# Kernel optimization log

Hardware: AMD Instinct MI355X
Metric: run time of the kernel (lower is better)

Reference implementation:

```python
import jax, jax.numpy as jnp
import numpy as np

NUM_HEADS = 32
NUM_KV_HEADS = 8
HEAD_DIM = 64
GQA_GROUPS = NUM_HEADS // NUM_KV_HEADS
HIDDEN = 2048
B, S = 2, 2048


def setup_inputs() -> dict:
    key = jax.random.key(0)
    ks = jax.random.split(key, 7)
    scale = 1.0 / np.sqrt(HIDDEN)
    return {
        "x": jax.random.normal(ks[0], (B, S, HIDDEN), dtype=jnp.float32),
        "rotary_cos": jax.random.uniform(ks[1], (S, HEAD_DIM // 2), dtype=jnp.float32),
        "rotary_sin": jax.random.uniform(ks[2], (S, HEAD_DIM // 2), dtype=jnp.float32),
        "Wq": jax.random.normal(ks[3], (HIDDEN, NUM_HEADS * HEAD_DIM), dtype=jnp.float32) * scale,
        "Wk": jax.random.normal(ks[4], (HIDDEN, NUM_KV_HEADS * HEAD_DIM), dtype=jnp.float32) * scale,
        "Wv": jax.random.normal(ks[5], (HIDDEN, NUM_KV_HEADS * HEAD_DIM), dtype=jnp.float32) * scale,
        "Wo": jax.random.normal(ks[6], (NUM_HEADS * HEAD_DIM, HIDDEN), dtype=jnp.float32) * scale,
    }


def _apply_rope(x, cos, sin):
    # x: (B, H, S, hd); cos/sin: (S, hd/2)
    d = x.shape[-1] // 2
    x1, x2 = x[..., :d], x[..., d:]
    cos = cos[None, None]  # (1,1,S,hd/2)
    sin = sin[None, None]
    return jnp.concatenate([x1 * cos - x2 * sin, x2 * cos + x1 * sin], axis=-1)


def reference(x, rotary_cos, rotary_sin, Wq, Wk, Wv, Wo):
    b, s, _ = x.shape
    scale = HEAD_DIM ** -0.5
    q = (x @ Wq).reshape(b, s, NUM_HEADS, HEAD_DIM).transpose(0, 2, 1, 3)
    k = (x @ Wk).reshape(b, s, NUM_KV_HEADS, HEAD_DIM).transpose(0, 2, 1, 3)
    v = (x @ Wv).reshape(b, s, NUM_KV_HEADS, HEAD_DIM).transpose(0, 2, 1, 3)
    q = _apply_rope(q, rotary_cos[:s], rotary_sin[:s])
    k = _apply_rope(k, rotary_cos[:s], rotary_sin[:s])
    # GQA: expand kv heads to full head count (repeat each kv head gqa_groups times)
    k = jnp.repeat(k, GQA_GROUPS, axis=1)  # (B, H, S, hd)
    v = jnp.repeat(v, GQA_GROUPS, axis=1)
    attn = jnp.einsum("bhqd,bhkd->bhqk", q, k) * scale
    causal = jnp.triu(jnp.full((s, s), -jnp.inf, dtype=attn.dtype), k=1)
    attn = attn + causal[None, None]
    attn = jax.nn.softmax(attn.astype(jnp.float32), axis=-1).astype(q.dtype)
    out = jnp.einsum("bhqk,bhkd->bhqd", attn, v)
    out = out.transpose(0, 2, 1, 3).reshape(b, s, NUM_HEADS * HEAD_DIM)
    return out @ Wo
```

## Files before the change

kernel.cpp:

```cpp
#include <hip/hip_runtime.h>
#include <cstdint>
#include <cstddef>


typedef _Float16 f16;
typedef _Float16 half8 __attribute__((ext_vector_type(8)));
typedef _Float16 half4 __attribute__((ext_vector_type(4)));
typedef float floatx4 __attribute__((ext_vector_type(4)));

#define NH 32
#define NKV 8
#define HD 64
#define BB 2
#define SS 2048
#define HID 2048

__device__ __forceinline__ float fast_exp2(float x) {
#if __has_builtin(__builtin_amdgcn_exp2f)
  return __builtin_amdgcn_exp2f(x);
#else
  return __expf(x * 0.69314718056f);
#endif
}

__device__ __forceinline__ void async_copy16(const f16* g, f16* l) {
  __builtin_amdgcn_global_load_lds(
      (const __attribute__((address_space(1))) void*)g,
      (__attribute__((address_space(3))) void*)l, 16, 0, 0);
}

__device__ __forceinline__ void transpose64(const float* __restrict__ in,
                                            f16* __restrict__ out,
                                            int C, int l, float* tile) {
  const int t = threadIdx.x;
  const int nx = C >> 6;
  const int c0 = (l % nx) * 64, r0 = (l / nx) * 64;
#pragma unroll
  for (int p = 0; p < 2; ++p) {
    const int idx = t + p * 512;
    const int r = idx >> 4, cf = (idx & 15) * 4;
    const float4 v = *(const float4*)(in + (size_t)(r0 + r) * C + c0 + cf);
    tile[r * 65 + cf + 0] = v.x; tile[r * 65 + cf + 1] = v.y;
    tile[r * 65 + cf + 2] = v.z; tile[r * 65 + cf + 3] = v.w;
  }
  __syncthreads();
  const int rp = t >> 3, k8 = (t & 7) * 8;
  half8 o;
#pragma unroll
  for (int j = 0; j < 8; ++j) o[j] = (f16)tile[(k8 + j) * 65 + rp];
  *(half8*)(out + (size_t)(c0 + rp) * 2048 + r0 + k8) = o;
  __syncthreads();
}

__global__ __launch_bounds__(512) void k_prep(const float* __restrict__ x,
                                              const float* __restrict__ Wq,
                                              const float* __restrict__ Wk,
                                              const float* __restrict__ Wv,
                                              f16* __restrict__ Xb,
                                              f16* __restrict__ WqT,
                                              f16* __restrict__ WkT,
                                              f16* __restrict__ WvT) {
  __shared__ float tile[64 * 65];
  const int bid = blockIdx.x;
  const int t = threadIdx.x;
  if (bid < 2048) {
    const size_t i = ((size_t)bid * 512 + t) * 8;
    const float4 a = *(const float4*)(x + i);
    const float4 b = *(const float4*)(x + i + 4);
    half8 h;
    h[0] = (f16)a.x; h[1] = (f16)a.y; h[2] = (f16)a.z; h[3] = (f16)a.w;
    h[4] = (f16)b.x; h[5] = (f16)b.y; h[6] = (f16)b.z; h[7] = (f16)b.w;
    *(half8*)(Xb + i) = h;
    return;
  }
  if (bid < 3072)      transpose64(Wq, WqT, 2048, bid - 2048, tile);
  else if (bid < 3328) transpose64(Wk, WkT, 512, bid - 3072, tile);
  else                 transpose64(Wv, WvT, 512, bid - 3328, tile);
}

__device__ __forceinline__ void core256(const f16* __restrict__ A,
                                        const f16* __restrict__ Bt,
                                        const int K, const int m0, const int n0,
                                        f16* __restrict__ SM,
                                        floatx4 (&acc)[8][4]) {
  const int t = threadIdx.x;
  const int w = t >> 6, lane = t & 63;
  const int wr = w >> 2, wc = w & 3;
  const int quad = lane >> 4, col = lane & 15;
  const int nkt = K >> 6;

  f16* const Ab0 = SM;
  f16* const Ab1 = SM + 16384;
  f16* const Bb0 = SM + 32768;
  f16* const Bb1 = SM + 49152;

  const int srow = t >> 3;
  const int schunk = (t & 7) ^ (srow & 7);
  const f16* const Asrc = A + (size_t)(m0 + srow) * K + schunk * 8;
  const f16* const Bsrc = Bt + (size_t)(n0 + srow) * K + schunk * 8;
  const int ldst = w * 512;

  const floatx4 zero = {0.f, 0.f, 0.f, 0.f};
#pragma unroll
  for (int i = 0; i < 8; ++i)
#pragma unroll
    for (int j = 0; j < 4; ++j) acc[i][j] = zero;

#pragma unroll
  for (int r = 0; r < 4; ++r)
    async_copy16(Asrc + (size_t)(r * 64) * K, Ab0 + r * 4096 + ldst);
#pragma unroll
  for (int r = 0; r < 4; ++r)
    async_copy16(Bsrc + (size_t)(r * 64) * K, Bb0 + r * 4096 + ldst);
  __asm__ volatile("s_waitcnt vmcnt(0)" ::: "memory");
  __builtin_amdgcn_s_barrier();

  for (int kt = 0; kt < nkt; ++kt) {
    const f16* const Ac = (kt & 1) ? Ab1 : Ab0;
    const f16* const Bc = (kt & 1) ? Bb1 : Bb0;
    f16* const An = (kt & 1) ? Ab0 : Ab1;
    f16* const Bn = (kt & 1) ? Bb0 : Bb1;
    const bool pf = (kt + 1 < nkt);
    const f16* const Apf = Asrc + (size_t)(kt + 1) * 64;
    const f16* const Bpf = Bsrc + (size_t)(kt + 1) * 64;
    half8 bf[4][2];
#pragma unroll
    for (int q = 0; q < 4; ++q) {
      if (q == 0) {
#pragma unroll
        for (int j = 0; j < 4; ++j) {
          const int rb = wc * 64 + j * 16 + col;
#pragma unroll
          for (int kc = 0; kc < 2; ++kc)
            bf[j][kc] = *(const half8*)(Bc + rb * 64 +
                                        (((kc * 4 + quad) ^ (rb & 7)) * 8));
        }
      }
      half8 af[2][2];
#pragma unroll
      for (int ii = 0; ii < 2; ++ii) {
        const int ra = wr * 128 + (q * 2 + ii) * 16 + col;
#pragma unroll
        for (int kc = 0; kc < 2; ++kc)
          af[ii][kc] = *(const half8*)(Ac + ra * 64 +
                                       (((kc * 4 + quad) ^ (ra & 7)) * 8));
      }
      if (pf) {
        if (q == 0) {
          async_copy16(Bpf, Bn + ldst);
          async_copy16(Bpf + (size_t)64 * K, Bn + 4096 + ldst);
        } else if (q == 1) {
          async_copy16(Bpf + (size_t)128 * K, Bn + 8192 + ldst);
          async_copy16(Bpf + (size_t)192 * K, Bn + 12288 + ldst);
        } else if (q == 2) {
          async_copy16(Apf, An + ldst);
          async_copy16(Apf + (size_t)128 * K, An + 8192 + ldst);
        } else {
          async_copy16(Apf + (size_t)64 * K, An + 4096 + ldst);
          async_copy16(Apf + (size_t)192 * K, An + 12288 + ldst);
        }
      }
      __builtin_amdgcn_s_barrier();
      __asm__ volatile("s_waitcnt lgkmcnt(0)" ::: "memory");
      __builtin_amdgcn_sched_barrier(0);
      __builtin_amdgcn_s_setprio(1);
#pragma unroll
      for (int ii = 0; ii < 2; ++ii)
#pragma unroll
        for (int j = 0; j < 4; ++j) {
          acc[q * 2 + ii][j] = __builtin_amdgcn_mfma_f32_16x16x32_f16(
              af[ii][0], bf[j][0], acc[q * 2 + ii][j], 0, 0, 0);
          acc[q * 2 + ii][j] = __builtin_amdgcn_mfma_f32_16x16x32_f16(
              af[ii][1], bf[j][1], acc[q * 2 + ii][j], 0, 0, 0);
        }
      __builtin_amdgcn_s_setprio(0);
      if (q == 1) {
        if (pf) __asm__ volatile("s_waitcnt vmcnt(4)" ::: "memory");
        else    __asm__ volatile("s_waitcnt vmcnt(0)" ::: "memory");
      }
      if (q == 3 && pf) {
        __asm__ volatile("s_waitcnt vmcnt(2)" ::: "memory");
      }
      __builtin_amdgcn_s_barrier();
    }
  }
}

__global__ __launch_bounds__(512, 2) void k_gemm_qkv(const f16* __restrict__ A,
                                                     const f16* __restrict__ Bt,
                                                     const float* __restrict__ rc,
                                                     const float* __restrict__ rs,
                                                     const float* __restrict__ Wo,
                                                     f16* __restrict__ WoT,
                                                     f16* __restrict__ Qr,
                                                     f16* __restrict__ Kr,
                                                     f16* __restrict__ Vt) {
  __shared__ f16 SM[65536];
  const int bid = blockIdx.x;
  if (bid >= 192) {
    float* tile = (float*)SM;
    const int l0 = (bid - 192) * 16;
#pragma unroll
    for (int it = 0; it < 16; ++it)
      transpose64(Wo, WoT, 2048, l0 + it, tile);
    return;
  }
  const int swz = (bid & 7) * 24 + (bid >> 3);
  const int nt = swz % 12, mt = swz / 12;
  const int m0 = mt * 256, n0 = nt * 256;

  floatx4 acc[8][4];
  core256(A, Bt, HID, m0, n0, SM, acc);

  const int t = threadIdx.x;
  const int w = t >> 6, lane = t & 63;
  const int wr = w >> 2, wc = w & 3;
  const int quad = lane >> 4, col = lane & 15;

  if (nt < 10) {
    f16* outp;
    int nheads, hh;
    float scale;
    if (nt < 8) { outp = Qr; nheads = NH; hh = (n0 + wc * 64) >> 6;
                  scale = 0.125f * 1.44269504089f; }
    else        { outp = Kr; nheads = NKV; hh = (n0 - 2048 + wc * 64) >> 6;
                  scale = 1.0f; }
#pragma unroll
    for (int i = 0; i < 8; ++i) {
#pragma unroll
      for (int r = 0; r < 4; ++r) {
        const int sg = m0 + wr * 128 + i * 16 + quad * 4 + r;
        const int b = sg >> 11, s = sg & 2047;
        const float c1 = rc[s * 32 + col];
        const float sv1 = rs[s * 32 + col];
        const float c2 = rc[s * 32 + 16 + col];
        const float sv2 = rs[s * 32 + 16 + col];
        f16* op = outp + ((size_t)(b * nheads + hh) * SS + s) * HD;
        const float x1a = acc[i][0][r], x2a = acc[i][2][r];
        op[col]      = (f16)((x1a * c1 - x2a * sv1) * scale);
        op[col + 32] = (f16)((x2a * c1 + x1a * sv1) * scale);
        const float x1b = acc[i][1][r], x2b = acc[i][3][r];
        op[col + 16] = (f16)((x1b * c2 - x2b * sv2) * scale);
        op[col + 48] = (f16)((x2b * c2 + x1b * sv2) * scale);
      }
    }
  } else {
    const int kv0 = (n0 - 2560) >> 6;
    const int bb = m0 >> 11;
    const int s0 = m0 & 2047;
#pragma unroll
    for (int hs = 0; hs < 2; ++hs) {
      __builtin_amdgcn_s_barrier();
      if (wr == hs) {
#pragma unroll
        for (int i = 0; i < 8; ++i)
#pragma unroll
          for (int j = 0; j < 4; ++j) {
            const int dl = wc * 64 + j * 16 + col;
            const int sl = i * 16 + quad * 4;
            half4 pv;
            pv[0] = (f16)acc[i][j][0]; pv[1] = (f16)acc[i][j][1];
            pv[2] = (f16)acc[i][j][2]; pv[3] = (f16)acc[i][j][3];
            *(half4*)(SM + dl * 136 + sl) = pv;
          }
      }
      __builtin_amdgcn_s_barrier();
#pragma unroll
      for (int rr = 0; rr < 8; ++rr) {
        const int flat = t + rr * 512;
        const int dl = flat >> 4, s8 = (flat & 15) * 8;
        const int kv = kv0 + (dl >> 6), d = dl & 63;
        f16* vp = Vt + ((size_t)(bb * NKV + kv) * HD + d) * SS + s0 +
                  hs * 128 + s8;
        *(uint4*)vp = *(const uint4*)(SM + dl * 136 + s8);
      }
    }
  }
}

__global__ __launch_bounds__(256) void k_gemm(const f16* __restrict__ A,
                                              const f16* __restrict__ Bt,
                                              float* __restrict__ Cf,
                                              int N, int K) {
  __shared__ f16 As[128 * 64];
  __shared__ f16 Bs[128 * 64];
  const int t = threadIdx.x;
  const int w = t >> 6, lane = t & 63;
  const int m0 = blockIdx.y * 128, n0 = blockIdx.x * 128;
  const int wm = (w >> 1) * 64, wn = (w & 1) * 64;
  const int quad = lane >> 4, col = lane & 15;
  const int srow = lane >> 3;
  const int schunk = (lane & 7) ^ srow;

  floatx4 acc[4][4];
  const floatx4 zero = {0.f, 0.f, 0.f, 0.f};
#pragma unroll
  for (int i = 0; i < 4; ++i)
#pragma unroll
    for (int j = 0; j < 4; ++j) acc[i][j] = zero;

  const f16* Ag = A + (size_t)(m0 + w * 32 + srow) * K + schunk * 8;
  const f16* Bg = Bt + (size_t)(n0 + w * 32 + srow) * K + schunk * 8;
  f16* Al = As + (w * 32) * 64;
  f16* Bl = Bs + (w * 32) * 64;

  for (int k0 = 0; k0 < K; k0 += 64) {
#pragma unroll
    for (int i = 0; i < 4; ++i) {
      async_copy16(Ag + k0 + (size_t)(i * 8) * K, Al + i * 8 * 64);
      async_copy16(Bg + k0 + (size_t)(i * 8) * K, Bl + i * 8 * 64);
    }
    __syncthreads();
    half8 af[2][4], bf[2][4];
#pragma unroll
    for (int kc = 0; kc < 2; ++kc)
#pragma unroll
      for (int i = 0; i < 4; ++i) {
        const int ra = wm + i * 16 + col;
        const int rb = wn + i * 16 + col;
        af[kc][i] = *(const half8*)(As + ra * 64 + ((kc * 4 + quad) ^ (ra & 7)) * 8);
        bf[kc][i] = *(const half8*)(Bs + rb * 64 + ((kc * 4 + quad) ^ (rb & 7)) * 8);
      }
#pragma unroll
    for (int i = 0; i < 4; ++i)
#pragma unroll
      for (int j = 0; j < 4; ++j) {
        acc[i][j] = __builtin_amdgcn_mfma_f32_16x16x32_f16(af[0][i], bf[0][j], acc[i][j], 0, 0, 0);
        acc[i][j] = __builtin_amdgcn_mfma_f32_16x16x32_f16(af[1][i], bf[1][j], acc[i][j], 0, 0, 0);
      }
    __syncthreads();
  }
#pragma unroll
  for (int i = 0; i < 4; ++i) {
    const int row0 = m0 + wm + i * 16 + quad * 4;
#pragma unroll
    for (int j = 0; j < 4; ++j) {
      const int cc = n0 + wn + j * 16 + col;
#pragma unroll
      for (int r = 0; r < 4; ++r)
        Cf[(size_t)(row0 + r) * N + cc] = acc[i][j][r];
    }
  }
}

__global__ __launch_bounds__(256, 2) void k_attn(const f16* __restrict__ Qb,
                                                 const f16* __restrict__ Kb,
                                                 const f16* __restrict__ Vg,
                                                 f16* __restrict__ O) {
  __shared__ f16 Ks[2][64 * 64];
  __shared__ f16 Vs[2][64 * 64];
  __shared__ f16 Pl[4][32 * 72];
  const int t = threadIdx.x;
  const int w = t >> 6, lane = t & 63;
  const int quad = lane >> 4, col = lane & 15;
  const int qp = blockIdx.x;
  const int kv = blockIdx.y, b = blockIdx.z;
  const int h = kv * 4 + w;
  f16* P = &Pl[w][0];

  const f16* Qh = Qb + (size_t)(b * NH + h) * SS * HD;
  const f16* Kh = Kb + (size_t)(b * NKV + kv) * SS * HD;
  const f16* Vh = Vg + (size_t)(b * NKV + kv) * HD * SS;

  int sr[2], sl[2];
#pragma unroll
  for (int j = 0; j < 2; ++j) {
    const int flat = t + j * 256;
    sr[j] = flat >> 3;
    sl[j] = (flat & 7) ^ (sr[j] & 7);
  }

  const int cx7 = col & 7;
  const floatx4 zero = {0.f, 0.f, 0.f, 0.f};
  const float M = 10.0f;

#pragma unroll
  for (int tile = 0; tile < 2; ++tile) {
    const int qt = tile ? qp : 63 - qp;
    const int qb = qt * 32;

    half8 qf[2][2];
#pragma unroll
    for (int rt = 0; rt < 2; ++rt)
#pragma unroll
      for (int kc = 0; kc < 2; ++kc)
        qf[rt][kc] = *(const half8*)(Qh + (size_t)(qb + rt * 16 + col) * HD + kc * 32 + quad * 8);

    floatx4 oacc[2][4];
#pragma unroll
    for (int rt = 0; rt < 2; ++rt)
#pragma unroll
      for (int dt = 0; dt < 4; ++dt) oacc[rt][dt] = zero;
    float lrow[2] = {0.f, 0.f};

    const int niter = (qb + 32 + 63) >> 6;

    __syncthreads();
#pragma unroll
    for (int j = 0; j < 2; ++j) {
      async_copy16(Kh + (size_t)sr[j] * HD + sl[j] * 8, &Ks[0][(t + j * 256) * 8]);
      async_copy16(Vh + (size_t)sr[j] * SS + sl[j] * 8, &Vs[0][(t + j * 256) * 8]);
    }

    for (int it = 0; it < niter; ++it) {
      const int kb0 = it << 6;
      __syncthreads();
      if (it + 1 < niter) {
        const int nb = (it + 1) & 1;
        const int kn = kb0 + 64;
#pragma unroll
        for (int j = 0; j < 2; ++j) {
          async_copy16(Kh + (size_t)(kn + sr[j]) * HD + sl[j] * 8, &Ks[nb][(t + j * 256) * 8]);
          async_copy16(Vh + (size_t)sr[j] * SS + kn + sl[j] * 8, &Vs[nb][(t + j * 256) * 8]);
        }
      }
      const f16* Kt = &Ks[it & 1][0];
      const f16* Vtl = &Vs[it & 1][0];

      half8 kf[4][2];
#pragma unroll
      for (int st = 0; st < 4; ++st)
#pragma unroll
        for (int kc = 0; kc < 2; ++kc)
          kf[st][kc] = *(const half8*)(Kt + (st * 16 + col) * 64 + (((kc * 4 + quad) ^ cx7) * 8));

      floatx4 s[2][4];
      __builtin_amdgcn_s_setprio(1);
#pragma unroll
      for (int rt = 0; rt < 2; ++rt)
#pragma unroll
        for (int st = 0; st < 4; ++st) {
          floatx4 a = __builtin_amdgcn_mfma_f32_16x16x32_f16(kf[st][0], qf[rt][0], zero, 0, 0, 0);
          s[rt][st]  = __builtin_amdgcn_mfma_f32_16x16x32_f16(kf[st][1], qf[rt][1], a, 0, 0, 0);
        }
      __builtin_amdgcn_s_setprio(0);

      if (it == niter - 1) {
#pragma unroll
        for (int rt = 0; rt < 2; ++rt) {
          const int qrow = qb + rt * 16 + col;
#pragma unroll
          for (int st = 0; st < 4; ++st)
#pragma unroll
            for (int r = 0; r < 4; ++r)
              if (kb0 + st * 16 + quad * 4 + r > qrow) s[rt][st][r] = -1e30f;
        }
      }

#pragma unroll
      for (int rt = 0; rt < 2; ++rt) {
        float psum = 0.f;
#pragma unroll
        for (int st = 0; st < 4; ++st) {
          const float p0 = fast_exp2(s[rt][st][0] - M);
          const float p1 = fast_exp2(s[rt][st][1] - M);
          const float p2 = fast_exp2(s[rt][st][2] - M);
          const float p3 = fast_exp2(s[rt][st][3] - M);
          psum += (p0 + p1) + (p2 + p3);
          half4 pk;
          pk[0] = (f16)p0; pk[1] = (f16)p1; pk[2] = (f16)p2; pk[3] = (f16)p3;
          *(half4*)(P + (rt * 16 + col) * 72 + st * 16 + quad * 4) = pk;
        }
        psum += __shfl_xor(psum, 16, 64);
        psum += __shfl_xor(psum, 32, 64);
        lrow[rt] += psum;
      }

      __asm__ volatile("s_waitcnt lgkmcnt(0)" ::: "memory");

      half8 vf[4][2], pf[2][2];
#pragma unroll
      for (int dt = 0; dt < 4; ++dt)
#pragma unroll
        for (int kc = 0; kc < 2; ++kc)
          vf[dt][kc] = *(const half8*)(Vtl + (dt * 16 + col) * 64 + (((kc * 4 + quad) ^ cx7) * 8));
#pragma unroll
      for (int rt = 0; rt < 2; ++rt) {
        pf[rt][0] = *(const half8*)(P + (rt * 16 + col) * 72 + quad * 8);
        pf[rt][1] = *(const half8*)(P + (rt * 16 + col) * 72 + 32 + quad * 8);
      }
      __builtin_amdgcn_s_setprio(1);
#pragma unroll
      for (int rt = 0; rt < 2; ++rt)
#pragma unroll
        for (int dt = 0; dt < 4; ++dt) {
          oacc[rt][dt] = __builtin_amdgcn_mfma_f32_16x16x32_f16(vf[dt][0], pf[rt][0], oacc[rt][dt], 0, 0, 0);
          oacc[rt][dt] = __builtin_amdgcn_mfma_f32_16x16x32_f16(vf[dt][1], pf[rt][1], oacc[rt][dt], 0, 0, 0);
        }
      __builtin_amdgcn_s_setprio(0);
    }

#pragma unroll
    for (int rt = 0; rt < 2; ++rt) {
      const float inv = 1.0f / lrow[rt];
      f16* op = O + (size_t)(b * SS + qb + rt * 16 + col) * 2048 + h * 64;
#pragma unroll
      for (int dt = 0; dt < 4; ++dt) {
        half4 ov;
        ov[0] = (f16)(oacc[rt][dt][0] * inv);
        ov[1] = (f16)(oacc[rt][dt][1] * inv);
        ov[2] = (f16)(oacc[rt][dt][2] * inv);
        ov[3] = (f16)(oacc[rt][dt][3] * inv);
        *(half4*)(op + dt * 16 + quad * 4) = ov;
      }
    }
  }
}

extern "C" void kernel_launch(void* const* d_in, const int* in_sizes, int n_in,
                              void* d_out, int out_size, void* d_ws, size_t ws_size,
                              hipStream_t stream) {
  const float* x  = (const float*)d_in[0];
  const float* rc = (const float*)d_in[1];
  const float* rs = (const float*)d_in[2];
  const float* Wq = (const float*)d_in[3];
  const float* Wk = (const float*)d_in[4];
  const float* Wv = (const float*)d_in[5];
  const float* Wo = (const float*)d_in[6];
  float* out = (float*)d_out;

  char* ws = (char*)d_ws;
  f16* Xb  = (f16*)(ws);
  f16* WqT = (f16*)(ws + 16777216);
  f16* WkT = (f16*)(ws + 25165824);
  f16* WvT = (f16*)(ws + 27262976);
  f16* WoT = (f16*)(ws + 29360128);
  f16* Qr  = (f16*)(ws + 62914560);
  f16* Kr  = (f16*)(ws + 79691776);
  f16* Vt  = (f16*)(ws + 83886080);
  f16* O   = Xb;

  k_prep<<<3584, 512, 0, stream>>>(x, Wq, Wk, Wv, Xb, WqT, WkT, WvT);
  k_gemm_qkv<<<256, 512, 0, stream>>>(Xb, WqT, rc, rs, Wo, WoT, Qr, Kr, Vt);
  k_attn<<<dim3(32, NKV, BB), 256, 0, stream>>>(Qr, Kr, Vt, O);
  k_gemm<<<dim3(16, 32), 256, 0, stream>>>(O, WoT, out, 2048, HID);
}
```

Measured before the change: 281.0 us.

## Process one 64-row query tile per attention block instead of paired 32-row tiles

```diff
diff --git a/kernel.cpp b/kernel.cpp
--- a/kernel.cpp
+++ b/kernel.cpp
@@ -349,7 +349,7 @@
                                                  f16* __restrict__ O) {
   __shared__ f16 Ks[2][64 * 64];
   __shared__ f16 Vs[2][64 * 64];
-  __shared__ f16 Pl[4][32 * 72];
+  __shared__ f16 Pl[4][64 * 72];
   const int t = threadIdx.x;
   const int w = t >> 6, lane = t & 63;
   const int quad = lane >> 4, col = lane & 15;
@@ -373,136 +373,124 @@
   const int cx7 = col & 7;
   const floatx4 zero = {0.f, 0.f, 0.f, 0.f};
   const float M = 10.0f;
-
-#pragma unroll
-  for (int tile = 0; tile < 2; ++tile) {
-    const int qt = tile ? qp : 63 - qp;
-    const int qb = qt * 32;
-
-    half8 qf[2][2];
-#pragma unroll
-    for (int rt = 0; rt < 2; ++rt)
+  const int qb = qp * 64;
+  const int niter = qp + 1;
+
+  half8 qf[4][2];
+#pragma unroll
+  for (int rt = 0; rt < 4; ++rt)
+#pragma unroll
+    for (int kc = 0; kc < 2; ++kc)
+      qf[rt][kc] = *(const half8*)(Qh + (size_t)(qb + rt * 16 + col) * HD + kc * 32 + quad * 8);
+
+  floatx4 oacc[4][4];
+#pragma unroll
+  for (int rt = 0; rt < 4; ++rt)
+#pragma unroll
+    for (int dt = 0; dt < 4; ++dt) oacc[rt][dt] = zero;
+  float lrow[4] = {0.f, 0.f, 0.f, 0.f};
+
+#pragma unroll
+  for (int j = 0; j < 2; ++j) {
+    async_copy16(Kh + (size_t)sr[j] * HD + sl[j] * 8, &Ks[0][(t + j * 256) * 8]);
+    async_copy16(Vh + (size_t)sr[j] * SS + sl[j] * 8, &Vs[0][(t + j * 256) * 8]);
+  }
+
+  for (int it = 0; it < niter; ++it) {
+    const int kb0 = it << 6;
+    __syncthreads();
+    if (it + 1 < niter) {
+      const int nb = (it + 1) & 1;
+      const int kn = kb0 + 64;
+#pragma unroll
+      for (int j = 0; j < 2; ++j) {
+        async_copy16(Kh + (size_t)(kn + sr[j]) * HD + sl[j] * 8, &Ks[nb][(t + j * 256) * 8]);
+        async_copy16(Vh + (size_t)sr[j] * SS + kn + sl[j] * 8, &Vs[nb][(t + j * 256) * 8]);
+      }
+    }
+    const f16* Kt = &Ks[it & 1][0];
+    const f16* Vtl = &Vs[it & 1][0];
+
+    half8 kf[4][2];
+#pragma unroll
+    for (int st = 0; st < 4; ++st)
 #pragma unroll
       for (int kc = 0; kc < 2; ++kc)
-        qf[rt][kc] = *(const half8*)(Qh + (size_t)(qb + rt * 16 + col) * HD + kc * 32 + quad * 8);
-
-    floatx4 oacc[2][4];
-#pragma unroll
-    for (int rt = 0; rt < 2; ++rt)
-#pragma unroll
-      for (int dt = 0; dt < 4; ++dt) oacc[rt][dt] = zero;
-    float lrow[2] = {0.f, 0.f};
-
-    const int niter = (qb + 32 + 63) >> 6;
-
-    __syncthreads();
-#pragma unroll
-    for (int j = 0; j < 2; ++j) {
-      async_copy16(Kh + (size_t)sr[j] * HD + sl[j] * 8, &Ks[0][(t + j * 256) * 8]);
-      async_copy16(Vh + (size_t)sr[j] * SS + sl[j] * 8, &Vs[0][(t + j * 256) * 8]);
-    }
-
-    for (int it = 0; it < niter; ++it) {
-      const int kb0 = it << 6;
-      __syncthreads();
-      if (it + 1 < niter) {
-        const int nb = (it + 1) & 1;
-        const int kn = kb0 + 64;
-#pragma unroll
-        for (int j = 0; j < 2; ++j) {
-          async_copy16(Kh + (size_t)(kn + sr[j]) * HD + sl[j] * 8, &Ks[nb][(t + j * 256) * 8]);
-          async_copy16(Vh + (size_t)sr[j] * SS + kn + sl[j] * 8, &Vs[nb][(t + j * 256) * 8]);
-        }
-      }
-      const f16* Kt = &Ks[it & 1][0];
-      const f16* Vtl = &Vs[it & 1][0];
-
-      half8 kf[4][2];
-#pragma unroll
-      for (int st = 0; st < 4; ++st)
-#pragma unroll
-        for (int kc = 0; kc < 2; ++kc)
-          kf[st][kc] = *(const half8*)(Kt + (st * 16 + col) * 64 + (((kc * 4 + quad) ^ cx7) * 8));
-
-      floatx4 s[2][4];
+        kf[st][kc] = *(const half8*)(Kt + (st * 16 + col) * 64 + (((kc * 4 + quad) ^ cx7) * 8));
+
+    const bool last = (it == niter - 1);
+#pragma unroll
+    for (int rt = 0; rt < 4; ++rt) {
+      floatx4 s[4];
       __builtin_amdgcn_s_setprio(1);
 #pragma unroll
-      for (int rt = 0; rt < 2; ++rt)
-#pragma unroll
-        for (int st = 0; st < 4; ++st) {
-          floatx4 a = __builtin_amdgcn_mfma_f32_16x16x32_f16(kf[st][0], qf[rt][0], zero, 0, 0, 0);
-          s[rt][st]  = __builtin_amdgcn_mfma_f32_16x16x32_f16(kf[st][1], qf[rt][1], a, 0, 0, 0);
-        }
+      for (int st = 0; st < 4; ++st) {
+        floatx4 a = __builtin_amdgcn_mfma_f32_16x16x32_f16(kf[st][0], qf[rt][0], zero, 0, 0, 0);
+        s[st]     = __builtin_amdgcn_mfma_f32_16x16x32_f16(kf[st][1], qf[rt][1], a, 0, 0, 0);
+      }
       __builtin_amdgcn_s_setprio(0);
-
-      if (it == niter - 1) {
-#pragma unroll
-        for (int rt = 0; rt < 2; ++rt) {
-          const int qrow = qb + rt * 16 + col;
-#pragma unroll
-          for (int st = 0; st < 4; ++st)
-#pragma unroll
-            for (int r = 0; r < 4; ++r)
-              if (kb0 + st * 16 + quad * 4 + r > qrow) s[rt][st][r] = -1e30f;
-        }
-      }
-
-#pragma unroll
-      for (int rt = 0; rt < 2; ++rt) {
-        float psum = 0.f;
-#pragma unroll
-        for (int st = 0; st < 4; ++st) {
-          const float p0 = fast_exp2(s[rt][st][0] - M);
-          const float p1 = fast_exp2(s[rt][st][1] - M);
-          const float p2 = fast_exp2(s[rt][st][2] - M);
-          const float p3 = fast_exp2(s[rt][st][3] - M);
-          psum += (p0 + p1) + (p2 + p3);
-          half4 pk;
-          pk[0] = (f16)p0; pk[1] = (f16)p1; pk[2] = (f16)p2; pk[3] = (f16)p3;
-          *(half4*)(P + (rt * 16 + col) * 72 + st * 16 + quad * 4) = pk;
-        }
-        psum += __shfl_xor(psum, 16, 64);
-        psum += __shfl_xor(psum, 32, 64);
-        lrow[rt] += psum;
-      }
-
-      __asm__ volatile("s_waitcnt lgkmcnt(0)" ::: "memory");
-
-      half8 vf[4][2], pf[2][2];
-#pragma unroll
-      for (int dt = 0; dt < 4; ++dt)
-#pragma unroll
-        for (int kc = 0; kc < 2; ++kc)
-          vf[dt][kc] = *(const half8*)(Vtl + (dt * 16 + col) * 64 + (((kc * 4 + quad) ^ cx7) * 8));
-#pragma unroll
-      for (int rt = 0; rt < 2; ++rt) {
-        pf[rt][0] = *(const half8*)(P + (rt * 16 + col) * 72 + quad * 8);
-        pf[rt][1] = *(const half8*)(P + (rt * 16 + col) * 72 + 32 + quad * 8);
-      }
-      __builtin_amdgcn_s_setprio(1);
-#pragma unroll
-      for (int rt = 0; rt < 2; ++rt)
-#pragma unroll
-        for (int dt = 0; dt < 4; ++dt) {
-          oacc[rt][dt] = __builtin_amdgcn_mfma_f32_16x16x32_f16(vf[dt][0], pf[rt][0], oacc[rt][dt], 0, 0, 0);
-          oacc[rt][dt] = __builtin_amdgcn_mfma_f32_16x16x32_f16(vf[dt][1], pf[rt][1], oacc[rt][dt], 0, 0, 0);
-        }
-      __builtin_amdgcn_s_setprio(0);
-    }
-
-#pragma unroll
-    for (int rt = 0; rt < 2; ++rt) {
-      const float inv = 1.0f / lrow[rt];
-      f16* op = O + (size_t)(b * SS + qb + rt * 16 + col) * 2048 + h * 64;
+      if (last) {
+        const int qrow = qb + rt * 16 + col;
+#pragma unroll
+        for (int st = 0; st < 4; ++st)
+#pragma unroll
+          for (int r = 0; r < 4; ++r)
+            if (kb0 + st * 16 + quad * 4 + r > qrow) s[st][r] = -1e30f;
+      }
+      float psum = 0.f;
+#pragma unroll
+      for (int st = 0; st < 4; ++st) {
+        const float p0 = fast_exp2(s[st][0] - M);
+        const float p1 = fast_exp2(s[st][1] - M);
+        const float p2 = fast_exp2(s[st][2] - M);
+        const float p3 = fast_exp2(s[st][3] - M);
+        psum += (p0 + p1) + (p2 + p3);
+        half4 pk;
+        pk[0] = (f16)p0; pk[1] = (f16)p1; pk[2] = (f16)p2; pk[3] = (f16)p3;
+        *(half4*)(P + (rt * 16 + col) * 72 + st * 16 + quad * 4) = pk;
+      }
+      psum += __shfl_xor(psum, 16, 64);
+      psum += __shfl_xor(psum, 32, 64);
+      lrow[rt] += psum;
+    }
+
+    __asm__ volatile("s_waitcnt lgkmcnt(0)" ::: "memory");
+
+    half8 vf[4][2];
+#pragma unroll
+    for (int dt = 0; dt < 4; ++dt)
+#pragma unroll
+      for (int kc = 0; kc < 2; ++kc)
+        vf[dt][kc] = *(const half8*)(Vtl + (dt * 16 + col) * 64 + (((kc * 4 + quad) ^ cx7) * 8));
+    half8 pf[4][2];
+#pragma unroll
+    for (int rt = 0; rt < 4; ++rt) {
+      pf[rt][0] = *(const half8*)(P + (rt * 16 + col) * 72 + quad * 8);
+      pf[rt][1] = *(const half8*)(P + (rt * 16 + col) * 72 + 32 + quad * 8);
+    }
+    __builtin_amdgcn_s_setprio(1);
+#pragma unroll
+    for (int rt = 0; rt < 4; ++rt)
 #pragma unroll
       for (int dt = 0; dt < 4; ++dt) {
-        half4 ov;
-        ov[0] = (f16)(oacc[rt][dt][0] * inv);
-        ov[1] = (f16)(oacc[rt][dt][1] * inv);
-        ov[2] = (f16)(oacc[rt][dt][2] * inv);
-        ov[3] = (f16)(oacc[rt][dt][3] * inv);
-        *(half4*)(op + dt * 16 + quad * 4) = ov;
-      }
+        oacc[rt][dt] = __builtin_amdgcn_mfma_f32_16x16x32_f16(vf[dt][0], pf[rt][0], oacc[rt][dt], 0, 0, 0);
+        oacc[rt][dt] = __builtin_amdgcn_mfma_f32_16x16x32_f16(vf[dt][1], pf[rt][1], oacc[rt][dt], 0, 0, 0);
+      }
+    __builtin_amdgcn_s_setprio(0);
+  }
+
+#pragma unroll
+  for (int rt = 0; rt < 4; ++rt) {
+    const float inv = 1.0f / lrow[rt];
+    f16* op = O + (size_t)(b * SS + qb + rt * 16 + col) * 2048 + h * 64;
+#pragma unroll
+    for (int dt = 0; dt < 4; ++dt) {
+      half4 ov;
+      ov[0] = (f16)(oacc[rt][dt][0] * inv);
+      ov[1] = (f16)(oacc[rt][dt][1] * inv);
+      ov[2] = (f16)(oacc[rt][dt][2] * inv);
+      ov[3] = (f16)(oacc[rt][dt][3] * inv);
+      *(half4*)(op + dt * 16 + quad * 4) = ov;
     }
   }
 }
```

New measurement: 307.2 us. 9.3% more time.
